# Kernel tuning notes

Measured on AMD Instinct MI355X. Metric: run time of the kernel, lower is better.

## Reference

```python
import jax, jax.numpy as jnp
import numpy as np

ROUTINGS = 3

def squash(s, axis=-1):
    mag_sq = jnp.sum(s * s, axis=axis, keepdims=True)
    mag = jnp.sqrt(mag_sq)
    return mag_sq / (1.0 + mag_sq) * (s / (mag + 1e-8))

def setup_inputs() -> dict:
    key = jax.random.key(0)
    k1, k2 = jax.random.split(key)
    B, I, Din, O, Dout = 256, 1152, 8, 10, 16
    x = jax.random.normal(k1, (B, I, Din), dtype=jnp.float32)
    weight = 0.01 * jax.random.normal(k2, (O, I, Dout, Din), dtype=jnp.float32)
    return {"x": x, "weight": weight}

def reference(x, weight):
    # x: [B, I, Din]; weight: [O, I, Dout, Din]
    # x_hat: [B, O, I, Dout]
    x_hat = jnp.einsum('oidc,bic->boid', weight, x)
    x_hat_det = jax.lax.stop_gradient(x_hat)
    B, O, I, _ = x_hat.shape
    b = jnp.zeros((B, O, I), dtype=x_hat.dtype)
    outputs = None
    for i in range(ROUTINGS):
        c = jax.nn.softmax(b, axis=1)  # softmax over output capsules
        if i == ROUTINGS - 1:
            outputs = squash(jnp.sum(c[:, :, :, None] * x_hat, axis=2, keepdims=True))
        else:
            outputs = squash(jnp.sum(c[:, :, :, None] * x_hat_det, axis=2, keepdims=True))
            b = b + jnp.sum(outputs * x_hat_det, axis=-1)
    return jnp.squeeze(outputs, axis=2)  # [B, O, Dout]
```

## Files before the change

### kernel.cpp

```cpp
#include <hip/hip_runtime.h>

#define BB   256
#define II   1152
#define OO   10
#define DOUT 16

using h2 = __fp16 __attribute__((ext_vector_type(2)));
using h4 = __fp16 __attribute__((ext_vector_type(4)));
using h8 = __fp16 __attribute__((ext_vector_type(8)));
#define H2V(v, a, b) __builtin_shufflevector((v), (v), (a), (b))
#define FD(a, b, c)  __builtin_amdgcn_fdot2((a), (b), (c), false)

typedef __attribute__((address_space(3))) uint32_t lds_u32_t;
typedef __attribute__((address_space(1))) const uint32_t glb_u32_t;

__device__ __forceinline__ void dma16(const __fp16* g, __fp16* l) {
  __builtin_amdgcn_global_load_lds((glb_u32_t*)g, (lds_u32_t*)l, 16, 0, 0);
}

__device__ __forceinline__ float dpp_add_xor1(float v) {
  int r = __builtin_amdgcn_mov_dpp(__float_as_int(v), 0xB1, 0xF, 0xF, true);
  return v + __int_as_float(r);
}
__device__ __forceinline__ float dpp_add_xor2(float v) {
  int r = __builtin_amdgcn_mov_dpp(__float_as_int(v), 0x4E, 0xF, 0xF, true);
  return v + __int_as_float(r);
}
__device__ __forceinline__ float swz_add_xor4(float v) {
  int r = __builtin_amdgcn_ds_swizzle(__float_as_int(v), 0x101F);
  return v + __int_as_float(r);
}

__global__ __launch_bounds__(256) void convert_kernel(
    const float* __restrict__ x, const float* __restrict__ w,
    __fp16* __restrict__ x16, __fp16* __restrict__ w16)
{
  const int bid = blockIdx.x;
  if (bid < 2880) {
    const int t = bid * 256 + threadIdx.x;
    const int e = t & 63;
    const int r = t >> 6;
    const int o = r / II;
    const int i = r - o * II;
    const float2 v2 = *(const float2*)(w + (size_t)r * 128 + e * 2);
    *(h2*)(w16 + ((size_t)i * 12 + o) * 128 + e * 2) =
        __builtin_amdgcn_cvt_pkrtz(v2.x, v2.y);
  } else {
    const size_t t = (size_t)(bid - 2880) * 256 + threadIdx.x;
    const float4 v4 = *(const float4*)(x + t * 4);
    const h2 a = __builtin_amdgcn_cvt_pkrtz(v4.x, v4.y);
    const h2 c = __builtin_amdgcn_cvt_pkrtz(v4.z, v4.w);
    *(h4*)(x16 + t * 4) = __builtin_shufflevector(a, c, 0, 1, 2, 3);
  }
}

template<int K>
__global__ __launch_bounds__(256, 4) void pass_kernel(
    const __fp16* __restrict__ x16,
    const __fp16* __restrict__ w16,
    const float* __restrict__ V,
    float* __restrict__ plane)
{
  const int tid  = threadIdx.x;
  const int lane = tid & 63;
  const int wv   = tid >> 6;
  const int dsub = lane & 7;
  const int bl   = lane >> 3;
  const int icg  = blockIdx.x & 31;
  const int bg   = blockIdx.x >> 5;
  const int b    = bg * 8 + bl;
  const int i0   = (icg * 4 + wv) * 9;

  __shared__ __fp16 wt[4][3 * 1536];
  __fp16* const wbuf = wt[wv];

  float Vr[OO][2];
  if (K >= 1) {
#pragma unroll
    for (int o = 0; o < OO; ++o) {
      const float2 v2 = *(const float2*)(V + ((size_t)b * OO + o) * DOUT + dsub * 2);
      Vr[o][0] = v2.x; Vr[o][1] = v2.y;
    }
  }

  float s[OO][2];
#pragma unroll
  for (int o = 0; o < OO; ++o) { s[o][0] = 0.f; s[o][1] = 0.f; }

  #define STAGE(i_, ofs_)                                                      \
    {                                                                          \
      const __fp16* gp = w16 + (size_t)(i_) * 1536 + lane * 8;                 \
      dma16(gp,        wbuf + (ofs_));                                         \
      dma16(gp + 512,  wbuf + (ofs_) + 512);                                   \
      dma16(gp + 1024, wbuf + (ofs_) + 1024);                                  \
    }

  const __fp16* xrow = x16 + ((size_t)b * II + i0) * 8;

  STAGE(i0, 0)
  h8 xq = *(const h8*)(xrow);
  asm volatile("" ::: "memory");
  STAGE(i0 + 1, 1536)
  h8 xn = *(const h8*)(xrow + 8);

  int cur = 0;
#pragma unroll 1
  for (int ii = 0; ii < 9; ++ii) {
    asm volatile("s_waitcnt vmcnt(4)" ::: "memory");
    __builtin_amdgcn_sched_barrier(0);

    const __fp16* wtb = wbuf + cur * 1536;
    const h2 xq0 = H2V(xq, 0, 1), xq1 = H2V(xq, 2, 3);
    const h2 xq2 = H2V(xq, 4, 5), xq3 = H2V(xq, 6, 7);

    float xh[OO][2];
    float t[OO];
#pragma unroll
    for (int o = 0; o < OO; ++o) {
      const __fp16* cp = wtb + (o * 16 + dsub * 2) * 8;
      const h8 wa = *(const h8*)(cp);
      const h8 wb = *(const h8*)(cp + 8);
      xh[o][0] = FD(H2V(wa, 0, 1), xq0, FD(H2V(wa, 2, 3), xq1,
                 FD(H2V(wa, 4, 5), xq2, FD(H2V(wa, 6, 7), xq3, 0.f))));
      xh[o][1] = FD(H2V(wb, 0, 1), xq0, FD(H2V(wb, 2, 3), xq1,
                 FD(H2V(wb, 4, 5), xq2, FD(H2V(wb, 6, 7), xq3, 0.f))));
      if (K >= 1)
        t[o] = Vr[o][0] * xh[o][0] + Vr[o][1] * xh[o][1];
    }

    if (K == 0) {
#pragma unroll
      for (int o = 0; o < OO; ++o) { s[o][0] += xh[o][0]; s[o][1] += xh[o][1]; }
    } else {
#pragma unroll
      for (int o = 0; o < OO; ++o) {
        t[o] = dpp_add_xor1(t[o]);
        t[o] = dpp_add_xor2(t[o]);
        t[o] = swz_add_xor4(t[o]);
      }
      float sum = 0.f;
#pragma unroll
      for (int o = 0; o < OO; ++o) { t[o] = __expf(t[o]); sum += t[o]; }
      const float inv = __builtin_amdgcn_rcpf(sum);
#pragma unroll
      for (int o = 0; o < OO; ++o) {
        const float c = t[o] * inv;
        s[o][0] += c * xh[o][0];
        s[o][1] += c * xh[o][1];
      }
    }

    const int inx = (ii < 7) ? (i0 + ii + 2) : (i0 + 8);
    int nbuf = cur - 1; if (nbuf < 0) nbuf += 3;
    STAGE(inx, nbuf * 1536)
    xq = xn;
    xn = *(const h8*)(x16 + ((size_t)b * II + inx) * 8);

    cur += 1; if (cur == 3) cur = 0;
  }
  #undef STAGE

  if (K == 0) {
#pragma unroll
    for (int o = 0; o < OO; ++o) { s[o][0] *= 0.1f; s[o][1] *= 0.1f; }
  }

  asm volatile("s_waitcnt vmcnt(0)" ::: "memory");
  if (wv != 0) {
    float* rr = (float*)&wt[wv][0] + bl * 168;
#pragma unroll
    for (int o = 0; o < OO; ++o)
      *(float2*)&rr[o * 16 + dsub * 2] = make_float2(s[o][0], s[o][1]);
  }
  __syncthreads();
  if (wv == 0) {
    float* out = plane + (size_t)b * (OO * DOUT);
#pragma unroll
    for (int o = 0; o < OO; ++o) {
      float a0 = s[o][0], a1 = s[o][1];
#pragma unroll
      for (int r = 1; r < 4; ++r) {
        const float2 v2 =
            *(const float2*)((const float*)&wt[r][0] + bl * 168 + o * 16 + dsub * 2);
        a0 += v2.x; a1 += v2.y;
      }
      unsafeAtomicAdd(&out[o * 16 + dsub * 2],     a0);
      unsafeAtomicAdd(&out[o * 16 + dsub * 2 + 1], a1);
    }
  }
}

template<int K>
__global__ __launch_bounds__(256) void reduce_kernel(
    const float* __restrict__ plane,
    float* __restrict__ V,
    float* __restrict__ out)
{
  const int idx = blockIdx.x * 256 + threadIdx.x;
  const float s = plane[idx];

  float sq = s * s;
  sq += __shfl_xor(sq, 1);
  sq += __shfl_xor(sq, 2);
  sq += __shfl_xor(sq, 4);
  sq += __shfl_xor(sq, 8);
  const float mag = sqrtf(sq);
  const float v = sq / (1.f + sq) * (s / (mag + 1e-8f));

  if (K == 0)      V[idx] = v;
  else if (K == 1) V[idx] += v;
  else             out[idx] = v;
}

extern "C" void kernel_launch(void* const* d_in, const int* in_sizes, int n_in,
                              void* d_out, int out_size, void* d_ws, size_t ws_size,
                              hipStream_t stream) {
  const float* x = (const float*)d_in[0];
  const float* w = (const float*)d_in[1];
  float* out = (float*)d_out;

  const size_t P = (size_t)BB * OO * DOUT;
  float* s0 = (float*)d_ws;
  float* s1 = s0 + P;
  float* s2 = s1 + P;
  float* V  = s2 + P;
  __fp16* x16 = (__fp16*)(V + P);
  __fp16* w16 = x16 + (size_t)BB * II * 8;

  hipMemsetAsync(s0, 0, 3 * P * sizeof(float), stream);
  convert_kernel<<<5184, 256, 0, stream>>>(x, w, x16, w16);

  const int pg = 1024;
  const int rg = (int)(P / 256);

  pass_kernel<0><<<pg, 256, 0, stream>>>(x16, w16, V, s0);
  reduce_kernel<0><<<rg, 256, 0, stream>>>(s0, V, out);
  pass_kernel<1><<<pg, 256, 0, stream>>>(x16, w16, V, s1);
  reduce_kernel<1><<<rg, 256, 0, stream>>>(s1, V, out);
  pass_kernel<2><<<pg, 256, 0, stream>>>(x16, w16, V, s2);
  reduce_kernel<2><<<rg, 256, 0, stream>>>(s2, V, out);
}
```

Measured before the change: 145.6 us.

## Fold squash of previous routing sums into pass kernels and batch LDS weight loads

Removes the two intermediate reduce kernels: each routing pass now reads the raw accumulated sums from earlier passes and recomputes the squash per lane with shuffles, building the agreement vector in registers. Only one final squash kernel remains, which cuts two launches and the V round-trip through global memory. The inner loop also issues all LDS weight loads for five output capsules before the dot products, separated by a scheduling barrier, to overlap LDS latency. The cost is redundant squash work in every block and higher register pressure from holding ten h8 weight vectors at once.

```diff
diff --git a/kernel.cpp b/kernel.cpp
--- a/kernel.cpp
+++ b/kernel.cpp
@@ -29,6 +29,18 @@
 __device__ __forceinline__ float swz_add_xor4(float v) {
   int r = __builtin_amdgcn_ds_swizzle(__float_as_int(v), 0x101F);
   return v + __int_as_float(r);
+}
+
+__device__ __forceinline__ void squash_pair(float v0, float v1,
+                                            float& o0, float& o1) {
+  float sq = v0 * v0 + v1 * v1;
+  sq += __shfl_xor(sq, 1);
+  sq += __shfl_xor(sq, 2);
+  sq += __shfl_xor(sq, 4);
+  const float mag = sqrtf(sq);
+  const float t1  = sq / (1.f + sq);
+  o0 = t1 * (v0 / (mag + 1e-8f));
+  o1 = t1 * (v1 / (mag + 1e-8f));
 }
 
 __global__ __launch_bounds__(256) void convert_kernel(
@@ -58,7 +70,8 @@
 __global__ __launch_bounds__(256, 4) void pass_kernel(
     const __fp16* __restrict__ x16,
     const __fp16* __restrict__ w16,
-    const float* __restrict__ V,
+    const float* __restrict__ r0,
+    const float* __restrict__ r1,
     float* __restrict__ plane)
 {
   const int tid  = threadIdx.x;
@@ -78,8 +91,16 @@
   if (K >= 1) {
 #pragma unroll
     for (int o = 0; o < OO; ++o) {
-      const float2 v2 = *(const float2*)(V + ((size_t)b * OO + o) * DOUT + dsub * 2);
-      Vr[o][0] = v2.x; Vr[o][1] = v2.y;
+      const float2 a = *(const float2*)(r0 + ((size_t)b * OO + o) * DOUT + dsub * 2);
+      float v0, v1;
+      squash_pair(a.x, a.y, v0, v1);
+      if (K == 2) {
+        const float2 c = *(const float2*)(r1 + ((size_t)b * OO + o) * DOUT + dsub * 2);
+        float u0, u1;
+        squash_pair(c.x, c.y, u0, u1);
+        v0 += u0; v1 += u1;
+      }
+      Vr[o][0] = v0; Vr[o][1] = v1;
     }
   }
 
@@ -96,7 +117,6 @@
     }
 
   const __fp16* xrow = x16 + ((size_t)b * II + i0) * 8;
-
   STAGE(i0, 0)
   h8 xq = *(const h8*)(xrow);
   asm volatile("" ::: "memory");
@@ -116,16 +136,25 @@
     float xh[OO][2];
     float t[OO];
 #pragma unroll
-    for (int o = 0; o < OO; ++o) {
-      const __fp16* cp = wtb + (o * 16 + dsub * 2) * 8;
-      const h8 wa = *(const h8*)(cp);
-      const h8 wb = *(const h8*)(cp + 8);
-      xh[o][0] = FD(H2V(wa, 0, 1), xq0, FD(H2V(wa, 2, 3), xq1,
-                 FD(H2V(wa, 4, 5), xq2, FD(H2V(wa, 6, 7), xq3, 0.f))));
-      xh[o][1] = FD(H2V(wb, 0, 1), xq0, FD(H2V(wb, 2, 3), xq1,
-                 FD(H2V(wb, 4, 5), xq2, FD(H2V(wb, 6, 7), xq3, 0.f))));
-      if (K >= 1)
-        t[o] = Vr[o][0] * xh[o][0] + Vr[o][1] * xh[o][1];
+    for (int half = 0; half < 2; ++half) {
+      h8 wz[10];
+      const __fp16* base = wtb + half * 640 + dsub * 16;
+#pragma unroll
+      for (int g = 0; g < 5; ++g) {
+        wz[2 * g]     = *(const h8*)(base + g * 128);
+        wz[2 * g + 1] = *(const h8*)(base + g * 128 + 8);
+      }
+      __builtin_amdgcn_sched_barrier(0);
+#pragma unroll
+      for (int g = 0; g < 5; ++g) {
+        const int o = half * 5 + g;
+        xh[o][0] = FD(H2V(wz[2*g], 0, 1), xq0, FD(H2V(wz[2*g], 2, 3), xq1,
+                   FD(H2V(wz[2*g], 4, 5), xq2, FD(H2V(wz[2*g], 6, 7), xq3, 0.f))));
+        xh[o][1] = FD(H2V(wz[2*g+1], 0, 1), xq0, FD(H2V(wz[2*g+1], 2, 3), xq1,
+                   FD(H2V(wz[2*g+1], 4, 5), xq2, FD(H2V(wz[2*g+1], 6, 7), xq3, 0.f))));
+        if (K >= 1)
+          t[o] = Vr[o][0] * xh[o][0] + Vr[o][1] * xh[o][1];
+      }
     }
 
     if (K == 0) {
@@ -174,26 +203,24 @@
   }
   __syncthreads();
   if (wv == 0) {
-    float* out = plane + (size_t)b * (OO * DOUT);
+    float* outp = plane + (size_t)b * (OO * DOUT);
 #pragma unroll
     for (int o = 0; o < OO; ++o) {
       float a0 = s[o][0], a1 = s[o][1];
 #pragma unroll
       for (int r = 1; r < 4; ++r) {
-        const float2 v2 =
-            *(const float2*)((const float*)&wt[r][0] + bl * 168 + o * 16 + dsub * 2);
+        const float2 v2 = *(const float2*)((const float*)&wt[r][0] +
+                                           bl * 168 + o * 16 + dsub * 2);
         a0 += v2.x; a1 += v2.y;
       }
-      unsafeAtomicAdd(&out[o * 16 + dsub * 2],     a0);
-      unsafeAtomicAdd(&out[o * 16 + dsub * 2 + 1], a1);
-    }
-  }
-}
-
-template<int K>
-__global__ __launch_bounds__(256) void reduce_kernel(
+      unsafeAtomicAdd(&outp[o * 16 + dsub * 2],     a0);
+      unsafeAtomicAdd(&outp[o * 16 + dsub * 2 + 1], a1);
+    }
+  }
+}
+
+__global__ __launch_bounds__(256) void final_kernel(
     const float* __restrict__ plane,
-    float* __restrict__ V,
     float* __restrict__ out)
 {
   const int idx = blockIdx.x * 256 + threadIdx.x;
@@ -205,11 +232,7 @@
   sq += __shfl_xor(sq, 4);
   sq += __shfl_xor(sq, 8);
   const float mag = sqrtf(sq);
-  const float v = sq / (1.f + sq) * (s / (mag + 1e-8f));
-
-  if (K == 0)      V[idx] = v;
-  else if (K == 1) V[idx] += v;
-  else             out[idx] = v;
+  out[idx] = sq / (1.f + sq) * (s / (mag + 1e-8f));
 }
 
 extern "C" void kernel_launch(void* const* d_in, const int* in_sizes, int n_in,
@@ -217,26 +240,23 @@
                               hipStream_t stream) {
   const float* x = (const float*)d_in[0];
   const float* w = (const float*)d_in[1];
-  float* out = (float*)d_out;
+  float* outp = (float*)d_out;
 
   const size_t P = (size_t)BB * OO * DOUT;
   float* s0 = (float*)d_ws;
   float* s1 = s0 + P;
   float* s2 = s1 + P;
-  float* V  = s2 + P;
-  __fp16* x16 = (__fp16*)(V + P);
+  __fp16* x16 = (__fp16*)(s2 + P);
   __fp16* w16 = x16 + (size_t)BB * II * 8;
 
   hipMemsetAsync(s0, 0, 3 * P * sizeof(float), stream);
   convert_kernel<<<5184, 256, 0, stream>>>(x, w, x16, w16);
 
   const int pg = 1024;
-  const int rg = (int)(P / 256);
-
-  pass_kernel<0><<<pg, 256, 0, stream>>>(x16, w16, V, s0);
-  reduce_kernel<0><<<rg, 256, 0, stream>>>(s0, V, out);
-  pass_kernel<1><<<pg, 256, 0, stream>>>(x16, w16, V, s1);
-  reduce_kernel<1><<<rg, 256, 0, stream>>>(s1, V, out);
-  pass_kernel<2><<<pg, 256, 0, stream>>>(x16, w16, V, s2);
-  reduce_kernel<2><<<rg, 256, 0, stream>>>(s2, V, out);
-}
+  const int fg = (int)(P / 256);
+
+  pass_kernel<0><<<pg, 256, 0, stream>>>(x16, w16, nullptr, nullptr, s0);
+  pass_kernel<1><<<pg, 256, 0, stream>>>(x16, w16, s0, nullptr, s1);
+  pass_kernel<2><<<pg, 256, 0, stream>>>(x16, w16, s0, s1, s2);
+  final_kernel<<<fg, 256, 0, stream>>>(s2, outp);
+}
```

Result: slower. 148.9 us (+2.3%).
